# Optimization experiments

Measured on AMD Instinct MI355X. Metric: run time of the kernel, lower is better.

Reference implementation:

```python
import jax, jax.numpy as jnp
import numpy as np

EPS = 1e-5


def conv1d(x, w, b):
    # x: (B, C_in, S), w: (C_out, C_in, K), 'same' padding = K//2
    pad = w.shape[-1] // 2
    y = jax.lax.conv_general_dilated(
        x, w, window_strides=(1,), padding=[(pad, pad)],
        dimension_numbers=("NCH", "OIH", "NCH"))
    return y + b[None, :, None]


def layer_norm(x, g, b):
    m = jnp.mean(x, axis=-1, keepdims=True)
    v = jnp.var(x, axis=-1, keepdims=True)
    return (x - m) * jax.lax.rsqrt(v + EPS) * g + b


def duration_predict(x, conv1_w, conv1_b, conv2_w, conv2_b,
                     ln1_g, ln1_b, ln2_g, ln2_b, lin_w, lin_b):
    # x: (B, S, C)
    out = conv1d(jnp.swapaxes(x, -2, -1), conv1_w, conv1_b)          # (B, F, S)
    out = jax.nn.relu(layer_norm(jnp.swapaxes(out, -2, -1), ln1_g, ln1_b))  # (B, S, F)
    out = conv1d(jnp.swapaxes(out, -2, -1), conv2_w, conv2_b)        # (B, F, S)
    out = jax.nn.relu(layer_norm(jnp.swapaxes(out, -2, -1), ln2_g, ln2_b))  # (B, S, F)
    out = jax.nn.relu(out @ lin_w.T + lin_b)                          # (B, S, 1)
    return jnp.squeeze(out, -1)                                       # (B, S)


def setup_inputs() -> dict:
    key = jax.random.key(0)
    ks = jax.random.split(key, 6)
    B, S, C = 16, 1024, 256
    F_, K = 256, 3
    inp = {
        "x": jax.random.normal(ks[0], (B, S, C), dtype=jnp.float32),
        "target": jax.random.uniform(ks[1], (B, S), dtype=jnp.float32),
        "conv1_w": jax.random.normal(ks[2], (F_, C, K), dtype=jnp.float32) * 0.02,
        "conv1_b": jnp.zeros((F_,), dtype=jnp.float32),
        "conv2_w": jax.random.normal(ks[3], (F_, F_, K), dtype=jnp.float32) * 0.02,
        "conv2_b": jnp.zeros((F_,), dtype=jnp.float32),
        "ln1_g": jnp.ones((F_,), dtype=jnp.float32),
        "ln1_b": jnp.zeros((F_,), dtype=jnp.float32),
        "ln2_g": jnp.ones((F_,), dtype=jnp.float32),
        "ln2_b": jnp.zeros((F_,), dtype=jnp.float32),
        "lin_w": jax.random.normal(ks[4], (1, F_), dtype=jnp.float32) * 0.02,
        "lin_b": jnp.zeros((1,), dtype=jnp.float32),
    }
    return inp


def reference(x, target, conv1_w, conv1_b, conv2_w, conv2_b,
              ln1_g, ln1_b, ln2_g, ln2_b, lin_w, lin_b):
    reg_len = duration_predict(x, conv1_w, conv1_b, conv2_w, conv2_b,
                               ln1_g, ln1_b, ln2_g, ln2_b, lin_w, lin_b)
    # Faithful to the original: max_len uses exp(target), the mask uses round(target).
    # max_len is data-dependent -> computed from concrete target (host-side, like the original).
    max_len = int(np.round(float(jnp.max(jnp.sum(jnp.exp(target), axis=-1)))))
    d = jnp.round(target)                 # (B, S) integer-valued durations (banker's rounding, like Python round)
    fin = jnp.cumsum(d, axis=-1)          # (B, S) end offsets
    start = fin - d                       # (B, S) start offsets
    t = jnp.arange(max_len, dtype=target.dtype)  # (T,)
    mask = ((t[None, None, :] >= start[..., None]) &
            (t[None, None, :] < fin[..., None])).astype(x.dtype)  # (B, S, T)
    # x.transpose @ mask -> (B, C, T) -> transpose -> (B, T, C)
    expanded = jnp.einsum("bsc,bst->btc", x, mask)
    return expanded, reg_len
```

## Files before the change

kernel.cpp:

```cpp
#include <hip/hip_runtime.h>
#include <hip/hip_bf16.h>

using frag_ab = __attribute__((ext_vector_type(8))) short;
using frag_cd = __attribute__((ext_vector_type(4))) float;

#define SLEN 1024
#define CDIM 256
#define KTOT 768
#define PD 8

static __device__ __forceinline__ short f2bf(float f) {
    __hip_bfloat16 h = __float2bfloat16(f);
    return *reinterpret_cast<short*>(&h);
}

__global__ __launch_bounds__(1024) void scan_scatter_kernel(
    const float* __restrict__ target, int* __restrict__ src, int T)
{
    const int b = blockIdx.x;
    const int tid = threadIdx.x;

    for (int i = tid; i < T; i += 1024) src[b * T + i] = -1;

    const float tv = target[b * SLEN + tid];
    const int d = (int)rintf(tv);

    const int lane = tid & 63;
    const int wid = tid >> 6;
    int v = d;
#pragma unroll
    for (int off = 1; off < 64; off <<= 1) {
        int n = __shfl_up(v, off);
        if (lane >= off) v += n;
    }
    __shared__ int waveSum[16];
    if (lane == 63) waveSum[wid] = v;
    __syncthreads();
    if (tid < 16) {
        int wv = waveSum[tid];
#pragma unroll
        for (int off = 1; off < 16; off <<= 1) {
            int n = __shfl_up(wv, off);
            if (tid >= off) wv += n;
        }
        waveSum[tid] = wv;
    }
    __syncthreads();
    const int fin = v + (wid > 0 ? waveSum[wid - 1] : 0);
    const int start = fin - d;
    for (int t = start; t < fin; ++t)
        if (t >= 0 && t < T) src[b * T + t] = tid;
}

__global__ __launch_bounds__(256) void expand_kernel(
    const float* __restrict__ x, const int* __restrict__ src,
    float* __restrict__ out, int T)
{
    const int row = blockIdx.x * 4 + (threadIdx.x >> 6);
    const int lane = threadIdx.x & 63;
    const int nrows = 16 * T;
    if (row >= nrows) return;
    const int b = row / T;
    const int s = src[row];
    float4 val = make_float4(0.f, 0.f, 0.f, 0.f);
    if (s >= 0)
        val = *(const float4*)(x + ((size_t)(b * SLEN + s)) * CDIM + lane * 4);
    *(float4*)(out + (size_t)row * CDIM + lane * 4) = val;
}

__global__ __launch_bounds__(256) void repack_w2(
    const float* __restrict__ w1, __hip_bfloat16* __restrict__ bt1,
    const float* __restrict__ w2, __hip_bfloat16* __restrict__ bt2)
{
    const int f = blockIdx.y;
    const int which = blockIdx.x / 3;
    const int K = (blockIdx.x % 3) * 256 + threadIdx.x;
    const int k3 = K >> 8;
    const int c = K & 255;
    const float* w = which ? w2 : w1;
    __hip_bfloat16* bt = which ? bt2 : bt1;
    bt[f * KTOT + K] = __float2bfloat16(w[f * KTOT + c * 3 + k3]);
}

__global__ __launch_bounds__(512, 2) void fused_conv(
    const float* __restrict__ x,
    const __hip_bfloat16* __restrict__ bt1,
    const __hip_bfloat16* __restrict__ bt2,
    const float* __restrict__ cb1, const float* __restrict__ g1, const float* __restrict__ be1,
    const float* __restrict__ cb2, const float* __restrict__ g2, const float* __restrict__ be2,
    const float* __restrict__ lw, const float* __restrict__ lb,
    float* __restrict__ reg_len)
{
    __shared__ __align__(16) unsigned char xt[68 * 512];
    __shared__ __align__(16) unsigned char yt[66 * 512];
    __shared__ float red[66][8][2];
    __shared__ float stats[66][2];

    const int tid = threadIdx.x;
    const int b = blockIdx.y;
    const int s0 = blockIdx.x * 64;

    const int lane = tid & 63;
    const int wid = tid >> 6;
    const int l15 = lane & 15;
    const int lk = lane >> 4;
    const int fbase = wid * 32;

    const __hip_bfloat16* p10 = bt1 + (size_t)(fbase + l15) * KTOT + lk * 8;
    const __hip_bfloat16* p11 = p10 + 16 * KTOT;
    frag_ab pb0[PD], pb1[PD];
#pragma unroll
    for (int i = 0; i < PD; ++i) {
        pb0[i] = *(const frag_ab*)(p10 + i * 32);
        pb1[i] = *(const frag_ab*)(p11 + i * 32);
    }

    const float* xin = x + (size_t)b * SLEN * CDIM;
    for (int ii = tid; ii < 68 * 32; ii += 512) {
        const int r = ii >> 5, cc = ii & 31;
        const int s = s0 - 2 + r;
        frag_ab v = {0, 0, 0, 0, 0, 0, 0, 0};
        if (s >= 0 && s < SLEN) {
            const float4* p = (const float4*)(xin + (size_t)s * CDIM + cc * 8);
            const float4 q0 = p[0], q1 = p[1];
            v[0] = f2bf(q0.x); v[1] = f2bf(q0.y); v[2] = f2bf(q0.z); v[3] = f2bf(q0.w);
            v[4] = f2bf(q1.x); v[5] = f2bf(q1.y); v[6] = f2bf(q1.z); v[7] = f2bf(q1.w);
        }
        *(frag_ab*)(xt + r * 512 + ((cc * 16) ^ ((r & 7) << 4))) = v;
    }
    __syncthreads();

    frag_cd acc1[5][2];
#pragma unroll
    for (int mf = 0; mf < 5; ++mf) {
        acc1[mf][0] = {0.f, 0.f, 0.f, 0.f};
        acc1[mf][1] = {0.f, 0.f, 0.f, 0.f};
    }
#pragma unroll
    for (int kk = 0; kk < 24; ++kk) {
        const frag_ab bb0 = pb0[kk % PD];
        const frag_ab bb1 = pb1[kk % PD];
        if (kk + PD < 24) {
            pb0[kk % PD] = *(const frag_ab*)(p10 + (kk + PD) * 32);
            pb1[kk % PD] = *(const frag_ab*)(p11 + (kk + PD) * 32);
        }
        const int k3 = kk >> 3;
        const int colbyte = (kk & 7) * 64 + lk * 16;
        frag_ab a[5];
#pragma unroll
        for (int mf = 0; mf < 5; ++mf) {
            int r = mf * 16 + l15 + k3;
            if (mf == 4) r = (r > 67) ? 67 : r;
            a[mf] = *(const frag_ab*)(xt + r * 512 + (colbyte ^ ((r & 7) << 4)));
        }
#pragma unroll
        for (int mf = 0; mf < 5; ++mf) {
            acc1[mf][0] = __builtin_amdgcn_mfma_f32_16x16x32_bf16(a[mf], bb0, acc1[mf][0], 0, 0, 0);
            acc1[mf][1] = __builtin_amdgcn_mfma_f32_16x16x32_bf16(a[mf], bb1, acc1[mf][1], 0, 0, 0);
        }
    }

    const __hip_bfloat16* p20 = bt2 + (size_t)(fbase + l15) * KTOT + lk * 8;
    const __hip_bfloat16* p21 = p20 + 16 * KTOT;
    frag_ab qb0[PD], qb1[PD];
#pragma unroll
    for (int i = 0; i < PD; ++i) {
        qb0[i] = *(const frag_ab*)(p20 + i * 32);
        qb1[i] = *(const frag_ab*)(p21 + i * 32);
    }

    {
        const float bias0 = cb1[fbase + l15];
        const float bias1 = cb1[fbase + 16 + l15];
#pragma unroll
        for (int mf = 0; mf < 5; ++mf) {
#pragma unroll
            for (int j = 0; j < 4; ++j) {
                acc1[mf][0][j] += bias0;
                acc1[mf][1][j] += bias1;
                float p = acc1[mf][0][j] + acc1[mf][1][j];
                float q = acc1[mf][0][j] * acc1[mf][0][j] + acc1[mf][1][j] * acc1[mf][1][j];
#pragma unroll
                for (int m = 1; m < 16; m <<= 1) {
                    p += __shfl_xor(p, m);
                    q += __shfl_xor(q, m);
                }
                const bool valid = (mf < 4) || (lk == 0 && j < 2);
                if (l15 == 0 && valid) {
                    const int yr = mf * 16 + lk * 4 + j;
                    red[yr][wid][0] = p;
                    red[yr][wid][1] = q;
                }
            }
        }
    }
    __syncthreads();
    if (tid < 66) {
        float s = 0.f, q = 0.f;
#pragma unroll
        for (int wv = 0; wv < 8; ++wv) { s += red[tid][wv][0]; q += red[tid][wv][1]; }
        const float mean = s * (1.f / 256.f);
        const float var = q * (1.f / 256.f) - mean * mean;
        stats[tid][0] = mean;
        stats[tid][1] = rsqrtf(var + 1e-5f);
    }
    __syncthreads();

    {
        const float ga0 = g1[fbase + l15], ga1 = g1[fbase + 16 + l15];
        const float bb0 = be1[fbase + l15], bb1 = be1[fbase + 16 + l15];
        const int c0b = (fbase + l15) * 2;
        const int c1b = (fbase + 16 + l15) * 2;
#pragma unroll
        for (int mf = 0; mf < 5; ++mf) {
#pragma unroll
            for (int j = 0; j < 4; ++j) {
                const bool valid = (mf < 4) || (lk == 0 && j < 2);
                if (valid) {
                    const int yr = mf * 16 + lk * 4 + j;
                    const float mean = stats[yr][0], rs = stats[yr][1];
                    const float v0 = fmaxf((acc1[mf][0][j] - mean) * rs * ga0 + bb0, 0.f);
                    const float v1 = fmaxf((acc1[mf][1][j] - mean) * rs * ga1 + bb1, 0.f);
                    const int sw = (yr & 7) << 4;
                    *(short*)(yt + yr * 512 + (c0b ^ sw)) = f2bf(v0);
                    *(short*)(yt + yr * 512 + (c1b ^ sw)) = f2bf(v1);
                }
            }
        }
    }
    __syncthreads();
    if (blockIdx.x == 0 && tid < 32) {
        frag_ab z = {0, 0, 0, 0, 0, 0, 0, 0};
        *(frag_ab*)(yt + (tid * 16)) = z;
    }
    if (blockIdx.x == 15 && tid >= 64 && tid < 96) {
        frag_ab z = {0, 0, 0, 0, 0, 0, 0, 0};
        const int cc = tid - 64;
        *(frag_ab*)(yt + 65 * 512 + ((cc * 16) ^ ((65 & 7) << 4))) = z;
    }
    __syncthreads();

    frag_cd acc2[4][2];
#pragma unroll
    for (int mf = 0; mf < 4; ++mf) {
        acc2[mf][0] = {0.f, 0.f, 0.f, 0.f};
        acc2[mf][1] = {0.f, 0.f, 0.f, 0.f};
    }
#pragma unroll
    for (int kk = 0; kk < 24; ++kk) {
        const frag_ab bb0 = qb0[kk % PD];
        const frag_ab bb1 = qb1[kk % PD];
        if (kk + PD < 24) {
            qb0[kk % PD] = *(const frag_ab*)(p20 + (kk + PD) * 32);
            qb1[kk % PD] = *(const frag_ab*)(p21 + (kk + PD) * 32);
        }
        const int k3 = kk >> 3;
        const int colbyte = (kk & 7) * 64 + lk * 16;
        frag_ab a[4];
#pragma unroll
        for (int mf = 0; mf < 4; ++mf) {
            const int r = mf * 16 + l15 + k3;
            a[mf] = *(const frag_ab*)(yt + r * 512 + (colbyte ^ ((r & 7) << 4)));
        }
#pragma unroll
        for (int mf = 0; mf < 4; ++mf) {
            acc2[mf][0] = __builtin_amdgcn_mfma_f32_16x16x32_bf16(a[mf], bb0, acc2[mf][0], 0, 0, 0);
            acc2[mf][1] = __builtin_amdgcn_mfma_f32_16x16x32_bf16(a[mf], bb1, acc2[mf][1], 0, 0, 0);
        }
    }

    {
        const float bias0 = cb2[fbase + l15];
        const float bias1 = cb2[fbase + 16 + l15];
#pragma unroll
        for (int mf = 0; mf < 4; ++mf) {
#pragma unroll
            for (int j = 0; j < 4; ++j) {
                acc2[mf][0][j] += bias0;
                acc2[mf][1][j] += bias1;
                float p = acc2[mf][0][j] + acc2[mf][1][j];
                float q = acc2[mf][0][j] * acc2[mf][0][j] + acc2[mf][1][j] * acc2[mf][1][j];
#pragma unroll
                for (int m = 1; m < 16; m <<= 1) {
                    p += __shfl_xor(p, m);
                    q += __shfl_xor(q, m);
                }
                if (l15 == 0) {
                    const int row = mf * 16 + lk * 4 + j;
                    red[row][wid][0] = p;
                    red[row][wid][1] = q;
                }
            }
        }
    }
    __syncthreads();
    if (tid < 64) {
        float s = 0.f, q = 0.f;
#pragma unroll
        for (int wv = 0; wv < 8; ++wv) { s += red[tid][wv][0]; q += red[tid][wv][1]; }
        const float mean = s * (1.f / 256.f);
        const float var = q * (1.f / 256.f) - mean * mean;
        stats[tid][0] = mean;
        stats[tid][1] = rsqrtf(var + 1e-5f);
    }
    __syncthreads();

    {
        const float ga0 = g2[fbase + l15], ga1 = g2[fbase + 16 + l15];
        const float bb0 = be2[fbase + l15], bb1 = be2[fbase + 16 + l15];
        const float lw0 = lw[fbase + l15], lw1 = lw[fbase + 16 + l15];
#pragma unroll
        for (int mf = 0; mf < 4; ++mf) {
#pragma unroll
            for (int j = 0; j < 4; ++j) {
                const int row = mf * 16 + lk * 4 + j;
                const float mean = stats[row][0], rs = stats[row][1];
                const float v0 = fmaxf((acc2[mf][0][j] - mean) * rs * ga0 + bb0, 0.f);
                const float v1 = fmaxf((acc2[mf][1][j] - mean) * rs * ga1 + bb1, 0.f);
                float p = v0 * lw0 + v1 * lw1;
#pragma unroll
                for (int m = 1; m < 16; m <<= 1) p += __shfl_xor(p, m);
                if (l15 == 0) red[row][wid][0] = p;
            }
        }
    }
    __syncthreads();
    if (tid < 64) {
        float s = 0.f;
#pragma unroll
        for (int wv = 0; wv < 8; ++wv) s += red[tid][wv][0];
        reg_len[b * SLEN + s0 + tid] = fmaxf(s + lb[0], 0.f);
    }
}

extern "C" void kernel_launch(void* const* d_in, const int* in_sizes, int n_in,
                              void* d_out, int out_size, void* d_ws, size_t ws_size,
                              hipStream_t stream)
{
    const float* x       = (const float*)d_in[0];
    const float* target  = (const float*)d_in[1];
    const float* conv1_w = (const float*)d_in[2];
    const float* conv1_b = (const float*)d_in[3];
    const float* conv2_w = (const float*)d_in[4];
    const float* conv2_b = (const float*)d_in[5];
    const float* ln1_g   = (const float*)d_in[6];
    const float* ln1_b   = (const float*)d_in[7];
    const float* ln2_g   = (const float*)d_in[8];
    const float* ln2_b   = (const float*)d_in[9];
    const float* lin_w   = (const float*)d_in[10];
    const float* lin_b   = (const float*)d_in[11];

    const int B = 16, S = 1024, C = 256;
    const int T = (out_size - B * S) / (B * C);

    float* expanded = (float*)d_out;
    float* reg_len  = (float*)d_out + (size_t)B * T * C;

    unsigned char* ws = (unsigned char*)d_ws;
    __hip_bfloat16* bt1 = (__hip_bfloat16*)ws;
    __hip_bfloat16* bt2 = (__hip_bfloat16*)(ws + 393216);
    int* src = (int*)(ws + 2 * 393216);

    scan_scatter_kernel<<<B, 1024, 0, stream>>>(target, src, T);
    repack_w2<<<dim3(6, 256), 256, 0, stream>>>(conv1_w, bt1, conv2_w, bt2);

    fused_conv<<<dim3(16, 16), 512, 0, stream>>>(
        x, bt1, bt2, conv1_b, ln1_g, ln1_b, conv2_b, ln2_g, ln2_b,
        lin_w, lin_b, reg_len);

    expand_kernel<<<(B * T + 3) / 4, 256, 0, stream>>>(x, src, expanded, T);
}
```

Measured before the change: 56.75 us.

## Halve sequence tile to 32 rows, doubling grid and raising occupancy

Each fused_conv block now handles 32 sequence positions instead of 64, so the grid grows from 256 to 512 blocks. This gives more parallelism across the 256 CUs, and with smaller LDS, fewer accumulators and a shallower weight prefetch depth the launch bound can target 4 blocks per SM. The tradeoff is more halo recomputation in conv1 (34 rows computed per 32 kept) and every block reloading the full weight matrices. Boundary zeroing of the conv1 output is folded into the LayerNorm write loop, which removes a barrier, and the reduction buffer is padded to avoid LDS bank conflicts.

Result: slower. 72.48 us (+27.7%).

```diff
diff --git a/kernel.cpp b/kernel.cpp
--- a/kernel.cpp
+++ b/kernel.cpp
@@ -7,7 +7,7 @@
 #define SLEN 1024
 #define CDIM 256
 #define KTOT 768
-#define PD 8
+#define PD 4
 
 static __device__ __forceinline__ short f2bf(float f) {
     __hip_bfloat16 h = __float2bfloat16(f);
@@ -82,7 +82,7 @@
     bt[f * KTOT + K] = __float2bfloat16(w[f * KTOT + c * 3 + k3]);
 }
 
-__global__ __launch_bounds__(512, 2) void fused_conv(
+__global__ __launch_bounds__(512, 4) void fused_conv(
     const float* __restrict__ x,
     const __hip_bfloat16* __restrict__ bt1,
     const __hip_bfloat16* __restrict__ bt2,
@@ -91,14 +91,14 @@
     const float* __restrict__ lw, const float* __restrict__ lb,
     float* __restrict__ reg_len)
 {
-    __shared__ __align__(16) unsigned char xt[68 * 512];
-    __shared__ __align__(16) unsigned char yt[66 * 512];
-    __shared__ float red[66][8][2];
-    __shared__ float stats[66][2];
+    __shared__ __align__(16) unsigned char xt[36 * 512];
+    __shared__ __align__(16) unsigned char yt[34 * 512];
+    __shared__ float red[34][17];
+    __shared__ float stats[34][2];
 
     const int tid = threadIdx.x;
     const int b = blockIdx.y;
-    const int s0 = blockIdx.x * 64;
+    const int s0 = blockIdx.x * 32;
 
     const int lane = tid & 63;
     const int wid = tid >> 6;
@@ -116,7 +116,7 @@
     }
 
     const float* xin = x + (size_t)b * SLEN * CDIM;
-    for (int ii = tid; ii < 68 * 32; ii += 512) {
+    for (int ii = tid; ii < 36 * 32; ii += 512) {
         const int r = ii >> 5, cc = ii & 31;
         const int s = s0 - 2 + r;
         frag_ab v = {0, 0, 0, 0, 0, 0, 0, 0};
@@ -130,9 +130,9 @@
     }
     __syncthreads();
 
-    frag_cd acc1[5][2];
-#pragma unroll
-    for (int mf = 0; mf < 5; ++mf) {
+    frag_cd acc1[3][2];
+#pragma unroll
+    for (int mf = 0; mf < 3; ++mf) {
         acc1[mf][0] = {0.f, 0.f, 0.f, 0.f};
         acc1[mf][1] = {0.f, 0.f, 0.f, 0.f};
     }
@@ -146,15 +146,15 @@
         }
         const int k3 = kk >> 3;
         const int colbyte = (kk & 7) * 64 + lk * 16;
-        frag_ab a[5];
-#pragma unroll
-        for (int mf = 0; mf < 5; ++mf) {
+        frag_ab a[3];
+#pragma unroll
+        for (int mf = 0; mf < 3; ++mf) {
             int r = mf * 16 + l15 + k3;
-            if (mf == 4) r = (r > 67) ? 67 : r;
+            if (mf == 2) r = (r > 35) ? 35 : r;
             a[mf] = *(const frag_ab*)(xt + r * 512 + (colbyte ^ ((r & 7) << 4)));
         }
 #pragma unroll
-        for (int mf = 0; mf < 5; ++mf) {
+        for (int mf = 0; mf < 3; ++mf) {
             acc1[mf][0] = __builtin_amdgcn_mfma_f32_16x16x32_bf16(a[mf], bb0, acc1[mf][0], 0, 0, 0);
             acc1[mf][1] = __builtin_amdgcn_mfma_f32_16x16x32_bf16(a[mf], bb1, acc1[mf][1], 0, 0, 0);
         }
@@ -173,7 +173,7 @@
         const float bias0 = cb1[fbase + l15];
         const float bias1 = cb1[fbase + 16 + l15];
 #pragma unroll
-        for (int mf = 0; mf < 5; ++mf) {
+        for (int mf = 0; mf < 3; ++mf) {
 #pragma unroll
             for (int j = 0; j < 4; ++j) {
                 acc1[mf][0][j] += bias0;
@@ -185,20 +185,20 @@
                     p += __shfl_xor(p, m);
                     q += __shfl_xor(q, m);
                 }
-                const bool valid = (mf < 4) || (lk == 0 && j < 2);
+                const bool valid = (mf < 2) || (lk == 0 && j < 2);
                 if (l15 == 0 && valid) {
                     const int yr = mf * 16 + lk * 4 + j;
-                    red[yr][wid][0] = p;
-                    red[yr][wid][1] = q;
+                    red[yr][wid * 2] = p;
+                    red[yr][wid * 2 + 1] = q;
                 }
             }
         }
     }
     __syncthreads();
-    if (tid < 66) {
+    if (tid < 34) {
         float s = 0.f, q = 0.f;
 #pragma unroll
-        for (int wv = 0; wv < 8; ++wv) { s += red[tid][wv][0]; q += red[tid][wv][1]; }
+        for (int wv = 0; wv < 8; ++wv) { s += red[tid][wv * 2]; q += red[tid][wv * 2 + 1]; }
         const float mean = s * (1.f / 256.f);
         const float var = q * (1.f / 256.f) - mean * mean;
         stats[tid][0] = mean;
@@ -212,15 +212,18 @@
         const int c0b = (fbase + l15) * 2;
         const int c1b = (fbase + 16 + l15) * 2;
 #pragma unroll
-        for (int mf = 0; mf < 5; ++mf) {
+        for (int mf = 0; mf < 3; ++mf) {
 #pragma unroll
             for (int j = 0; j < 4; ++j) {
-                const bool valid = (mf < 4) || (lk == 0 && j < 2);
+                const bool valid = (mf < 2) || (lk == 0 && j < 2);
                 if (valid) {
                     const int yr = mf * 16 + lk * 4 + j;
                     const float mean = stats[yr][0], rs = stats[yr][1];
-                    const float v0 = fmaxf((acc1[mf][0][j] - mean) * rs * ga0 + bb0, 0.f);
-                    const float v1 = fmaxf((acc1[mf][1][j] - mean) * rs * ga1 + bb1, 0.f);
+                    float v0 = fmaxf((acc1[mf][0][j] - mean) * rs * ga0 + bb0, 0.f);
+                    float v1 = fmaxf((acc1[mf][1][j] - mean) * rs * ga1 + bb1, 0.f);
+                    const bool zrow = (blockIdx.x == 0 && yr == 0) ||
+                                      (blockIdx.x == 31 && yr == 33);
+                    if (zrow) { v0 = 0.f; v1 = 0.f; }
                     const int sw = (yr & 7) << 4;
                     *(short*)(yt + yr * 512 + (c0b ^ sw)) = f2bf(v0);
                     *(short*)(yt + yr * 512 + (c1b ^ sw)) = f2bf(v1);
@@ -229,20 +232,10 @@
         }
     }
     __syncthreads();
-    if (blockIdx.x == 0 && tid < 32) {
-        frag_ab z = {0, 0, 0, 0, 0, 0, 0, 0};
-        *(frag_ab*)(yt + (tid * 16)) = z;
-    }
-    if (blockIdx.x == 15 && tid >= 64 && tid < 96) {
-        frag_ab z = {0, 0, 0, 0, 0, 0, 0, 0};
-        const int cc = tid - 64;
-        *(frag_ab*)(yt + 65 * 512 + ((cc * 16) ^ ((65 & 7) << 4))) = z;
-    }
-    __syncthreads();
-
-    frag_cd acc2[4][2];
-#pragma unroll
-    for (int mf = 0; mf < 4; ++mf) {
+
+    frag_cd acc2[2][2];
+#pragma unroll
+    for (int mf = 0; mf < 2; ++mf) {
         acc2[mf][0] = {0.f, 0.f, 0.f, 0.f};
         acc2[mf][1] = {0.f, 0.f, 0.f, 0.f};
     }
@@ -256,14 +249,14 @@
         }
         const int k3 = kk >> 3;
         const int colbyte = (kk & 7) * 64 + lk * 16;
-        frag_ab a[4];
-#pragma unroll
-        for (int mf = 0; mf < 4; ++mf) {
+        frag_ab a[2];
+#pragma unroll
+        for (int mf = 0; mf < 2; ++mf) {
             const int r = mf * 16 + l15 + k3;
             a[mf] = *(const frag_ab*)(yt + r * 512 + (colbyte ^ ((r & 7) << 4)));
         }
 #pragma unroll
-        for (int mf = 0; mf < 4; ++mf) {
+        for (int mf = 0; mf < 2; ++mf) {
             acc2[mf][0] = __builtin_amdgcn_mfma_f32_16x16x32_bf16(a[mf], bb0, acc2[mf][0], 0, 0, 0);
             acc2[mf][1] = __builtin_amdgcn_mfma_f32_16x16x32_bf16(a[mf], bb1, acc2[mf][1], 0, 0, 0);
         }
@@ -273,7 +266,7 @@
         const float bias0 = cb2[fbase + l15];
         const float bias1 = cb2[fbase + 16 + l15];
 #pragma unroll
-        for (int mf = 0; mf < 4; ++mf) {
+        for (int mf = 0; mf < 2; ++mf) {
 #pragma unroll
             for (int j = 0; j < 4; ++j) {
                 acc2[mf][0][j] += bias0;
@@ -287,17 +280,17 @@
                 }
                 if (l15 == 0) {
                     const int row = mf * 16 + lk * 4 + j;
-                    red[row][wid][0] = p;
-                    red[row][wid][1] = q;
+                    red[row][wid * 2] = p;
+                    red[row][wid * 2 + 1] = q;
                 }
             }
         }
     }
     __syncthreads();
-    if (tid < 64) {
+    if (tid < 32) {
         float s = 0.f, q = 0.f;
 #pragma unroll
-        for (int wv = 0; wv < 8; ++wv) { s += red[tid][wv][0]; q += red[tid][wv][1]; }
+        for (int wv = 0; wv < 8; ++wv) { s += red[tid][wv * 2]; q += red[tid][wv * 2 + 1]; }
         const float mean = s * (1.f / 256.f);
         const float var = q * (1.f / 256.f) - mean * mean;
         stats[tid][0] = mean;
@@ -310,7 +303,7 @@
         const float bb0 = be2[fbase + l15], bb1 = be2[fbase + 16 + l15];
         const float lw0 = lw[fbase + l15], lw1 = lw[fbase + 16 + l15];
 #pragma unroll
-        for (int mf = 0; mf < 4; ++mf) {
+        for (int mf = 0; mf < 2; ++mf) {
 #pragma unroll
             for (int j = 0; j < 4; ++j) {
                 const int row = mf * 16 + lk * 4 + j;
@@ -320,15 +313,15 @@
                 float p = v0 * lw0 + v1 * lw1;
 #pragma unroll
                 for (int m = 1; m < 16; m <<= 1) p += __shfl_xor(p, m);
-                if (l15 == 0) red[row][wid][0] = p;
+                if (l15 == 0) red[row][wid * 2] = p;
             }
         }
     }
     __syncthreads();
-    if (tid < 64) {
+    if (tid < 32) {
         float s = 0.f;
 #pragma unroll
-        for (int wv = 0; wv < 8; ++wv) s += red[tid][wv][0];
+        for (int wv = 0; wv < 8; ++wv) s += red[tid][wv * 2];
         reg_len[b * SLEN + s0 + tid] = fmaxf(s + lb[0], 0.f);
     }
 }
@@ -364,7 +357,7 @@
     scan_scatter_kernel<<<B, 1024, 0, stream>>>(target, src, T);
     repack_w2<<<dim3(6, 256), 256, 0, stream>>>(conv1_w, bt1, conv2_w, bt2);
 
-    fused_conv<<<dim3(16, 16), 512, 0, stream>>>(
+    fused_conv<<<dim3(32, 16), 512, 0, stream>>>(
         x, bt1, bt2, conv1_b, ln1_g, ln1_b, conv2_b, ln2_g, ln2_b,
         lin_w, lin_b, reg_len);
 
```

## Split conv K-dimension across two wave groups and merge scan with weight repack

Applied to the files above, without the earlier changes.

The fused conv kernel now runs 1024 threads per block, with two groups of 8 waves each taking half of the K reduction. Partial accumulators are combined through LDS scratch before the layer-norm epilogue, and the boundary-row zeroing moves into the epilogue. The scan/scatter and weight-repack kernels are merged into one launch to remove a kernel launch. Prefetch depth is halved to reduce register pressure, at the cost of extra LDS traffic and barriers, plus idle waves during the epilogues.

Measured after the change: 74.30 us. +30.9%, slower.

```diff
diff --git a/kernel.cpp b/kernel.cpp
--- a/kernel.cpp
+++ b/kernel.cpp
@@ -7,49 +7,64 @@
 #define SLEN 1024
 #define CDIM 256
 #define KTOT 768
-#define PD 8
+#define PD 4
 
 static __device__ __forceinline__ short f2bf(float f) {
     __hip_bfloat16 h = __float2bfloat16(f);
     return *reinterpret_cast<short*>(&h);
 }
 
-__global__ __launch_bounds__(1024) void scan_scatter_kernel(
-    const float* __restrict__ target, int* __restrict__ src, int T)
+__global__ __launch_bounds__(1024) void scan_repack_kernel(
+    const float* __restrict__ target, int* __restrict__ src, int T,
+    const float* __restrict__ w1, __hip_bfloat16* __restrict__ bt1,
+    const float* __restrict__ w2, __hip_bfloat16* __restrict__ bt2)
 {
-    const int b = blockIdx.x;
+    __shared__ int waveSum[16];
     const int tid = threadIdx.x;
 
-    for (int i = tid; i < T; i += 1024) src[b * T + i] = -1;
-
-    const float tv = target[b * SLEN + tid];
-    const int d = (int)rintf(tv);
-
-    const int lane = tid & 63;
-    const int wid = tid >> 6;
-    int v = d;
-#pragma unroll
-    for (int off = 1; off < 64; off <<= 1) {
-        int n = __shfl_up(v, off);
-        if (lane >= off) v += n;
-    }
-    __shared__ int waveSum[16];
-    if (lane == 63) waveSum[wid] = v;
-    __syncthreads();
-    if (tid < 16) {
-        int wv = waveSum[tid];
-#pragma unroll
-        for (int off = 1; off < 16; off <<= 1) {
-            int n = __shfl_up(wv, off);
-            if (tid >= off) wv += n;
-        }
-        waveSum[tid] = wv;
-    }
-    __syncthreads();
-    const int fin = v + (wid > 0 ? waveSum[wid - 1] : 0);
-    const int start = fin - d;
-    for (int t = start; t < fin; ++t)
-        if (t >= 0 && t < T) src[b * T + t] = tid;
+    if (blockIdx.x < 16) {
+        const int b = blockIdx.x;
+        for (int i = tid; i < T; i += 1024) src[b * T + i] = -1;
+
+        const float tv = target[b * SLEN + tid];
+        const int d = (int)rintf(tv);
+
+        const int lane = tid & 63;
+        const int wid = tid >> 6;
+        int v = d;
+#pragma unroll
+        for (int off = 1; off < 64; off <<= 1) {
+            int n = __shfl_up(v, off);
+            if (lane >= off) v += n;
+        }
+        if (lane == 63) waveSum[wid] = v;
+        __syncthreads();
+        if (tid < 16) {
+            int wv = waveSum[tid];
+#pragma unroll
+            for (int off = 1; off < 16; off <<= 1) {
+                int n = __shfl_up(wv, off);
+                if (tid >= off) wv += n;
+            }
+            waveSum[tid] = wv;
+        }
+        __syncthreads();
+        const int fin = v + (wid > 0 ? waveSum[wid - 1] : 0);
+        const int start = fin - d;
+        for (int t = start; t < fin; ++t)
+            if (t >= 0 && t < T) src[b * T + t] = tid;
+    } else {
+        const int id = (blockIdx.x - 16) * 1024 + tid;
+        const int which = id >= 196608;
+        const int e = which ? id - 196608 : id;
+        const int f = e / KTOT;
+        const int K = e - f * KTOT;
+        const int k3 = K >> 8;
+        const int c = K & 255;
+        const float* w = which ? w2 : w1;
+        __hip_bfloat16* bt = which ? bt2 : bt1;
+        bt[f * KTOT + K] = __float2bfloat16(w[f * KTOT + c * 3 + k3]);
+    }
 }
 
 __global__ __launch_bounds__(256) void expand_kernel(
@@ -68,21 +83,7 @@
     *(float4*)(out + (size_t)row * CDIM + lane * 4) = val;
 }
 
-__global__ __launch_bounds__(256) void repack_w2(
-    const float* __restrict__ w1, __hip_bfloat16* __restrict__ bt1,
-    const float* __restrict__ w2, __hip_bfloat16* __restrict__ bt2)
-{
-    const int f = blockIdx.y;
-    const int which = blockIdx.x / 3;
-    const int K = (blockIdx.x % 3) * 256 + threadIdx.x;
-    const int k3 = K >> 8;
-    const int c = K & 255;
-    const float* w = which ? w2 : w1;
-    __hip_bfloat16* bt = which ? bt2 : bt1;
-    bt[f * KTOT + K] = __float2bfloat16(w[f * KTOT + c * 3 + k3]);
-}
-
-__global__ __launch_bounds__(512, 2) void fused_conv(
+__global__ __launch_bounds__(1024, 1) void fused_conv(
     const float* __restrict__ x,
     const __hip_bfloat16* __restrict__ bt1,
     const __hip_bfloat16* __restrict__ bt2,
@@ -91,10 +92,12 @@
     const float* __restrict__ lw, const float* __restrict__ lb,
     float* __restrict__ reg_len)
 {
-    __shared__ __align__(16) unsigned char xt[68 * 512];
-    __shared__ __align__(16) unsigned char yt[66 * 512];
-    __shared__ float red[66][8][2];
-    __shared__ float stats[66][2];
+    __shared__ __align__(16) unsigned char lds[74752];
+    float (*red)[17]  = (float (*)[17])lds;
+    float (*stats)[2] = (float (*)[2])(lds + 4488);
+    unsigned char* xt  = lds + 5120;
+    unsigned char* yt  = lds + 39936;
+    unsigned char* scr = lds + 5120;
 
     const int tid = threadIdx.x;
     const int b = blockIdx.y;
@@ -104,19 +107,22 @@
     const int wid = tid >> 6;
     const int l15 = lane & 15;
     const int lk = lane >> 4;
-    const int fbase = wid * 32;
+    const int kg = wid >> 3;
+    const int w8 = wid & 7;
+    const int fbase = w8 * 32;
+    const int kbeg = kg * 12, kend = kbeg + 12;
 
     const __hip_bfloat16* p10 = bt1 + (size_t)(fbase + l15) * KTOT + lk * 8;
     const __hip_bfloat16* p11 = p10 + 16 * KTOT;
     frag_ab pb0[PD], pb1[PD];
 #pragma unroll
     for (int i = 0; i < PD; ++i) {
-        pb0[i] = *(const frag_ab*)(p10 + i * 32);
-        pb1[i] = *(const frag_ab*)(p11 + i * 32);
+        pb0[i] = *(const frag_ab*)(p10 + (kbeg + i) * 32);
+        pb1[i] = *(const frag_ab*)(p11 + (kbeg + i) * 32);
     }
 
     const float* xin = x + (size_t)b * SLEN * CDIM;
-    for (int ii = tid; ii < 68 * 32; ii += 512) {
+    for (int ii = tid; ii < 68 * 32; ii += 1024) {
         const int r = ii >> 5, cc = ii & 31;
         const int s = s0 - 2 + r;
         frag_ab v = {0, 0, 0, 0, 0, 0, 0, 0};
@@ -137,12 +143,13 @@
         acc1[mf][1] = {0.f, 0.f, 0.f, 0.f};
     }
 #pragma unroll
-    for (int kk = 0; kk < 24; ++kk) {
-        const frag_ab bb0 = pb0[kk % PD];
-        const frag_ab bb1 = pb1[kk % PD];
-        if (kk + PD < 24) {
-            pb0[kk % PD] = *(const frag_ab*)(p10 + (kk + PD) * 32);
-            pb1[kk % PD] = *(const frag_ab*)(p11 + (kk + PD) * 32);
+    for (int kk0 = 0; kk0 < 12; ++kk0) {
+        const int kk = kbeg + kk0;
+        const frag_ab bb0 = pb0[kk & 3];
+        const frag_ab bb1 = pb1[kk & 3];
+        if (kk + PD < kend) {
+            pb0[kk & 3] = *(const frag_ab*)(p10 + (kk + PD) * 32);
+            pb1[kk & 3] = *(const frag_ab*)(p11 + (kk + PD) * 32);
         }
         const int k3 = kk >> 3;
         const int colbyte = (kk & 7) * 64 + lk * 16;
@@ -165,11 +172,38 @@
     frag_ab qb0[PD], qb1[PD];
 #pragma unroll
     for (int i = 0; i < PD; ++i) {
-        qb0[i] = *(const frag_ab*)(p20 + i * 32);
-        qb1[i] = *(const frag_ab*)(p21 + i * 32);
-    }
-
-    {
+        qb0[i] = *(const frag_ab*)(p20 + (kbeg + i) * 32);
+        qb1[i] = *(const frag_ab*)(p21 + (kbeg + i) * 32);
+    }
+
+    __syncthreads();
+
+    if (kg == 1) {
+#pragma unroll
+        for (int mf = 0; mf < 5; ++mf) {
+            if (mf < 4 || lk == 0) {
+#pragma unroll
+                for (int n = 0; n < 2; ++n) {
+                    const int ch = fbase + n * 16 + l15;
+                    const int yr0 = mf * 16 + lk * 4;
+                    *(frag_cd*)(scr + ch * 272 + yr0 * 4) = acc1[mf][n];
+                }
+            }
+        }
+    }
+    __syncthreads();
+    if (kg == 0) {
+#pragma unroll
+        for (int mf = 0; mf < 5; ++mf) {
+            if (mf < 4 || lk == 0) {
+#pragma unroll
+                for (int n = 0; n < 2; ++n) {
+                    const int ch = fbase + n * 16 + l15;
+                    const int yr0 = mf * 16 + lk * 4;
+                    acc1[mf][n] += *(const frag_cd*)(scr + ch * 272 + yr0 * 4);
+                }
+            }
+        }
         const float bias0 = cb1[fbase + l15];
         const float bias1 = cb1[fbase + 16 + l15];
 #pragma unroll
@@ -188,8 +222,8 @@
                 const bool valid = (mf < 4) || (lk == 0 && j < 2);
                 if (l15 == 0 && valid) {
                     const int yr = mf * 16 + lk * 4 + j;
-                    red[yr][wid][0] = p;
-                    red[yr][wid][1] = q;
+                    red[yr][w8 * 2] = p;
+                    red[yr][w8 * 2 + 1] = q;
                 }
             }
         }
@@ -198,7 +232,7 @@
     if (tid < 66) {
         float s = 0.f, q = 0.f;
 #pragma unroll
-        for (int wv = 0; wv < 8; ++wv) { s += red[tid][wv][0]; q += red[tid][wv][1]; }
+        for (int wv = 0; wv < 8; ++wv) { s += red[tid][wv * 2]; q += red[tid][wv * 2 + 1]; }
         const float mean = s * (1.f / 256.f);
         const float var = q * (1.f / 256.f) - mean * mean;
         stats[tid][0] = mean;
@@ -206,7 +240,7 @@
     }
     __syncthreads();
 
-    {
+    if (kg == 0) {
         const float ga0 = g1[fbase + l15], ga1 = g1[fbase + 16 + l15];
         const float bb0 = be1[fbase + l15], bb1 = be1[fbase + 16 + l15];
         const int c0b = (fbase + l15) * 2;
@@ -219,8 +253,11 @@
                 if (valid) {
                     const int yr = mf * 16 + lk * 4 + j;
                     const float mean = stats[yr][0], rs = stats[yr][1];
-                    const float v0 = fmaxf((acc1[mf][0][j] - mean) * rs * ga0 + bb0, 0.f);
-                    const float v1 = fmaxf((acc1[mf][1][j] - mean) * rs * ga1 + bb1, 0.f);
+                    float v0 = fmaxf((acc1[mf][0][j] - mean) * rs * ga0 + bb0, 0.f);
+                    float v1 = fmaxf((acc1[mf][1][j] - mean) * rs * ga1 + bb1, 0.f);
+                    const bool zrow = (blockIdx.x == 0 && yr == 0) ||
+                                      (blockIdx.x == 15 && yr == 65);
+                    if (zrow) { v0 = 0.f; v1 = 0.f; }
                     const int sw = (yr & 7) << 4;
                     *(short*)(yt + yr * 512 + (c0b ^ sw)) = f2bf(v0);
                     *(short*)(yt + yr * 512 + (c1b ^ sw)) = f2bf(v1);
@@ -229,16 +266,6 @@
         }
     }
     __syncthreads();
-    if (blockIdx.x == 0 && tid < 32) {
-        frag_ab z = {0, 0, 0, 0, 0, 0, 0, 0};
-        *(frag_ab*)(yt + (tid * 16)) = z;
-    }
-    if (blockIdx.x == 15 && tid >= 64 && tid < 96) {
-        frag_ab z = {0, 0, 0, 0, 0, 0, 0, 0};
-        const int cc = tid - 64;
-        *(frag_ab*)(yt + 65 * 512 + ((cc * 16) ^ ((65 & 7) << 4))) = z;
-    }
-    __syncthreads();
 
     frag_cd acc2[4][2];
 #pragma unroll
@@ -247,12 +274,13 @@
         acc2[mf][1] = {0.f, 0.f, 0.f, 0.f};
     }
 #pragma unroll
-    for (int kk = 0; kk < 24; ++kk) {
-        const frag_ab bb0 = qb0[kk % PD];
-        const frag_ab bb1 = qb1[kk % PD];
-        if (kk + PD < 24) {
-            qb0[kk % PD] = *(const frag_ab*)(p20 + (kk + PD) * 32);
-            qb1[kk % PD] = *(const frag_ab*)(p21 + (kk + PD) * 32);
+    for (int kk0 = 0; kk0 < 12; ++kk0) {
+        const int kk = kbeg + kk0;
+        const frag_ab bb0 = qb0[kk & 3];
+        const frag_ab bb1 = qb1[kk & 3];
+        if (kk + PD < kend) {
+            qb0[kk & 3] = *(const frag_ab*)(p20 + (kk + PD) * 32);
+            qb1[kk & 3] = *(const frag_ab*)(p21 + (kk + PD) * 32);
         }
         const int k3 = kk >> 3;
         const int colbyte = (kk & 7) * 64 + lk * 16;
@@ -269,7 +297,30 @@
         }
     }
 
-    {
+    __syncthreads();
+
+    if (kg == 1) {
+#pragma unroll
+        for (int mf = 0; mf < 4; ++mf) {
+#pragma unroll
+            for (int n = 0; n < 2; ++n) {
+                const int ch = fbase + n * 16 + l15;
+                const int yr0 = mf * 16 + lk * 4;
+                *(frag_cd*)(scr + ch * 272 + yr0 * 4) = acc2[mf][n];
+            }
+        }
+    }
+    __syncthreads();
+    if (kg == 0) {
+#pragma unroll
+        for (int mf = 0; mf < 4; ++mf) {
+#pragma unroll
+            for (int n = 0; n < 2; ++n) {
+                const int ch = fbase + n * 16 + l15;
+                const int yr0 = mf * 16 + lk * 4;
+                acc2[mf][n] += *(const frag_cd*)(scr + ch * 272 + yr0 * 4);
+            }
+        }
         const float bias0 = cb2[fbase + l15];
         const float bias1 = cb2[fbase + 16 + l15];
 #pragma unroll
@@ -287,8 +338,8 @@
                 }
                 if (l15 == 0) {
                     const int row = mf * 16 + lk * 4 + j;
-                    red[row][wid][0] = p;
-                    red[row][wid][1] = q;
+                    red[row][w8 * 2] = p;
+                    red[row][w8 * 2 + 1] = q;
                 }
             }
         }
@@ -297,7 +348,7 @@
     if (tid < 64) {
         float s = 0.f, q = 0.f;
 #pragma unroll
-        for (int wv = 0; wv < 8; ++wv) { s += red[tid][wv][0]; q += red[tid][wv][1]; }
+        for (int wv = 0; wv < 8; ++wv) { s += red[tid][wv * 2]; q += red[tid][wv * 2 + 1]; }
         const float mean = s * (1.f / 256.f);
         const float var = q * (1.f / 256.f) - mean * mean;
         stats[tid][0] = mean;
@@ -305,7 +356,7 @@
     }
     __syncthreads();
 
-    {
+    if (kg == 0) {
         const float ga0 = g2[fbase + l15], ga1 = g2[fbase + 16 + l15];
         const float bb0 = be2[fbase + l15], bb1 = be2[fbase + 16 + l15];
         const float lw0 = lw[fbase + l15], lw1 = lw[fbase + 16 + l15];
@@ -320,7 +371,7 @@
                 float p = v0 * lw0 + v1 * lw1;
 #pragma unroll
                 for (int m = 1; m < 16; m <<= 1) p += __shfl_xor(p, m);
-                if (l15 == 0) red[row][wid][0] = p;
+                if (l15 == 0) red[row][w8 * 2] = p;
             }
         }
     }
@@ -328,7 +379,7 @@
     if (tid < 64) {
         float s = 0.f;
 #pragma unroll
-        for (int wv = 0; wv < 8; ++wv) s += red[tid][wv][0];
+        for (int wv = 0; wv < 8; ++wv) s += red[tid][wv * 2];
         reg_len[b * SLEN + s0 + tid] = fmaxf(s + lb[0], 0.f);
     }
 }
@@ -361,10 +412,10 @@
     __hip_bfloat16* bt2 = (__hip_bfloat16*)(ws + 393216);
     int* src = (int*)(ws + 2 * 393216);
 
-    scan_scatter_kernel<<<B, 1024, 0, stream>>>(target, src, T);
-    repack_w2<<<dim3(6, 256), 256, 0, stream>>>(conv1_w, bt1, conv2_w, bt2);
-
-    fused_conv<<<dim3(16, 16), 512, 0, stream>>>(
+    scan_repack_kernel<<<400, 1024, 0, stream>>>(
+        target, src, T, conv1_w, bt1, conv2_w, bt2);
+
+    fused_conv<<<dim3(16, 16), 1024, 0, stream>>>(
         x, bt1, bt2, conv1_b, ln1_g, ln1_b, conv2_b, ln2_g, ln2_b,
         lin_w, lin_b, reg_len);
 
```
